# Optimization experiments

Hardware: AMD Instinct MI355X
Metric: run time of the kernel (lower is better)

## Reference

```python
import jax, jax.numpy as jnp
import numpy as np

B, N, H, F, DIN, NC = 4, 1024, 8, 256, 256, 10  # batch graphs, nodes, heads, feat/head, input dim, classes


def setup_inputs() -> dict:
    key = jax.random.key(0)
    ks = jax.random.split(key, 12)
    def rn(k, shape, s=0.05):
        return jax.random.normal(k, shape, jnp.float32) * s
    return dict(
        features=rn(ks[0], (B, N, DIN), 1.0),
        eigvects=rn(ks[1], (B, N, DIN), 1.0),  # unused by forward, mirrors original signature
        attn_mask=jnp.zeros((B, N, N), jnp.float32),  # additive mask: 0 = edge, -inf = no edge
        W1=rn(ks[2], (DIN, H * F)), a_src1=rn(ks[3], (H, F)), a_tgt1=rn(ks[4], (H, F)),
        skip1=rn(ks[5], (DIN, H * F)), b1=jnp.zeros((H * F,), jnp.float32),
        W2=rn(ks[6], (H * F, H * F)), a_src2=rn(ks[7], (H, F)), a_tgt2=rn(ks[8], (H, F)),
        skip2=rn(ks[9], (H * F, H * F)), b2=jnp.zeros((F,), jnp.float32),
        Wc=rn(ks[10], (F, NC)), bc=jnp.zeros((NC,), jnp.float32),
    )


def _gat_layer(x, mask, W, a_s, a_t, skipW, b, concat):
    # GAT IMP2: dense all-pairs scores + additive connectivity mask. Dropout is eval-mode identity.
    Bb, Nn, _ = x.shape
    Hh, Ff = a_s.shape
    p = (x @ W).reshape(Bb, Nn, Hh, Ff)                      # projected node features (B,N,H,F)
    s_src = jnp.einsum('bnhf,hf->bnh', p, a_s)
    s_tgt = jnp.einsum('bnhf,hf->bnh', p, a_t)
    # score[b,i,j,h] = leaky(src_i + tgt_j) + mask[b,i,j]
    scores = jax.nn.leaky_relu(s_src[:, :, None, :] + s_tgt[:, None, :, :], 0.2) + mask[..., None]
    attn = jax.nn.softmax(scores, axis=2)                    # softmax over neighbors j
    out = jnp.einsum('bijh,bjhf->bihf', attn, p)
    out = out + (x @ skipW).reshape(Bb, Nn, Hh, Ff)          # skip connection (projected)
    out = out.reshape(Bb, Nn, Hh * Ff) if concat else out.mean(axis=2)
    out = out + b
    return jax.nn.elu(out) if concat else out


def reference(features, eigvects, attn_mask, W1, a_src1, a_tgt1, skip1, b1,
              W2, a_src2, a_tgt2, skip2, b2, Wc, bc):
    x = _gat_layer(features, attn_mask, W1, a_src1, a_tgt1, skip1, b1, True)   # (B,N,H*F), ELU
    x = _gat_layer(x, attn_mask, W2, a_src2, a_tgt2, skip2, b2, False)         # (B,N,F), heads averaged
    g = x.mean(axis=1)                                                         # mean pool over nodes
    return g @ Wc + bc                                                         # (B, n_classes)
```

## Files before the change

### kernel.cpp

```cpp
#include <hip/hip_runtime.h>
#include <hip/hip_bf16.h>
#include <stdint.h>
#include <stddef.h>

typedef __hip_bfloat16 bf16;
typedef __attribute__((ext_vector_type(8))) short bhalf8;
typedef __attribute__((ext_vector_type(4))) short short4v;
typedef __attribute__((ext_vector_type(4))) float floatx4;

static __device__ __forceinline__ float b2f(bf16 v) { return __bfloat162float(v); }
static __device__ __forceinline__ bf16  f2b(float v) { return __float2bfloat16(v); }
static __device__ __forceinline__ short f2s(float v) {
    union { bf16 b; short s; } u; u.b = __float2bfloat16(v); return u.s;
}
static __device__ __forceinline__ float s2f(short v) {
    union { short s; bf16 b; } u; u.s = v; return b2f(u.b);
}

static __device__ __forceinline__ float loadf(const void* p, size_t i, int f32) {
    return f32 ? ((const float*)p)[i] : b2f(((const bf16*)p)[i]);
}

static __device__ __forceinline__ void gl_lds16(const void* g, void* l) {
    __builtin_amdgcn_global_load_lds(
        (const __attribute__((address_space(1))) void*)g,
        (__attribute__((address_space(3))) void*)l, 16, 0, 0);
}

static __device__ __forceinline__ void load_mask4b(const bf16* m, size_t idx,
                                                   float* mv) {
    short4v v = *(const short4v*)(m + idx);
    #pragma unroll
    for (int t = 0; t < 4; t++) mv[t] = s2f(v[t]);
}

__global__ __launch_bounds__(256) void prep_k(const void* __restrict__ feat,
                                              bf16* __restrict__ featc,
                                              const void* __restrict__ mask,
                                              bf16* __restrict__ maskb,
                                              float* __restrict__ zbase, int nzero,
                                              const void* __restrict__ W1,
                                              bf16* __restrict__ W1t,
                                              const void* __restrict__ skip1,
                                              bf16* __restrict__ S1t,
                                              const void* __restrict__ W2,
                                              const void* __restrict__ a_src1,
                                              const void* __restrict__ a_tgt1,
                                              const void* __restrict__ a_src2,
                                              const void* __restrict__ a_tgt2,
                                              bf16* __restrict__ Wa1b,
                                              bf16* __restrict__ Wa2b,
                                              int* __restrict__ flagp)
{
    __shared__ int sflag;
    __shared__ bf16 tile[32][33];
    const int tid = threadIdx.x;

    if (tid < 64) {
        const unsigned short* s = (const unsigned short*)W1;
        int bad = 0;
        #pragma unroll
        for (int i = 0; i < 4; i++) {
            int e = (s[tid * 4 + i] >> 7) & 0xFF;
            if (e > 0x85 || (e != 0 && e < 0x60)) bad++;
        }
        bad += __shfl_xor(bad, 1, 64);
        bad += __shfl_xor(bad, 2, 64);
        bad += __shfl_xor(bad, 4, 64);
        bad += __shfl_xor(bad, 8, 64);
        bad += __shfl_xor(bad, 16, 64);
        bad += __shfl_xor(bad, 32, 64);
        if (tid == 0) sflag = (bad > 16) ? 1 : 0;
    }
    __syncthreads();
    const int f32 = sflag;

    int id = blockIdx.x;
    if (id == 0 && tid == 0) *flagp = f32;

    if (id < 4096) {
        const int i = id * 256 + tid;
        featc[i] = f32 ? f2b(((const float*)feat)[i]) : ((const bf16*)feat)[i];
        return;
    }
    id -= 4096;
    if (id < 4096) {
        const size_t i = (size_t)id * 1024 + tid * 4;
        if (f32) {
            float4 v = *(const float4*)((const float*)mask + i);
            short4v o;
            o[0] = f2s(v.x); o[1] = f2s(v.y); o[2] = f2s(v.z); o[3] = f2s(v.w);
            *(short4v*)(maskb + i) = o;
        } else {
            *(short4v*)(maskb + i) = *(const short4v*)((const bf16*)mask + i);
        }
        return;
    }
    id -= 4096;
    if (id < 480) {
        const int i = id * 256 + tid;
        if (i < nzero) zbase[i] = 0.f;
        return;
    }
    id -= 480;
    if (id < 1024) {
        const void* in = (id < 512) ? W1 : skip1;
        bf16* out = (id < 512) ? W1t : S1t;
        const int t = id & 511;
        const int bx = t & 63, byy = t >> 6;
        const int tx = tid & 31, ty = tid >> 5;
        const int c0 = bx * 32, r0 = byy * 32;
        #pragma unroll
        for (int yy = ty; yy < 32; yy += 8)
            tile[yy][tx] = f2b(loadf(in, (size_t)(r0 + yy) * 2048 + c0 + tx, f32));
        __syncthreads();
        #pragma unroll
        for (int yy = ty; yy < 32; yy += 8)
            out[(size_t)(c0 + yy) * 256 + r0 + tx] = tile[tx][yy];
        return;
    }
    id -= 1024;
    if (id < 512) {
        const int wave = tid >> 6, lane = tid & 63;
        const int base = id * 64;
        const int hh = base >> 11, h = hh & 7;
        const void* a = (hh < 8) ? a_src2 : a_tgt2;
        float av[4];
        #pragma unroll
        for (int i = 0; i < 4; i++) av[i] = loadf(a, h * 256 + lane * 4 + i, f32);
        #pragma unroll 4
        for (int o = 0; o < 16; o++) {
            const int idx = base + wave * 16 + o;
            const int k = idx & 2047;
            float acc = 0.f;
            #pragma unroll
            for (int i = 0; i < 4; i++)
                acc = fmaf(loadf(W2, (size_t)k * 2048 + h * 256 + lane * 4 + i, f32),
                           av[i], acc);
            #pragma unroll
            for (int off2 = 32; off2; off2 >>= 1) acc += __shfl_down(acc, off2, 64);
            if (lane == 0) Wa2b[idx] = f2b(acc);
        }
        return;
    }
    id -= 512;
    {
        const int wave = tid >> 6, lane = tid & 63;
        const int base = id * 64;
        const int hh = base >> 8, h = hh & 7;
        const void* a = (hh < 8) ? a_src1 : a_tgt1;
        float av[4];
        #pragma unroll
        for (int i = 0; i < 4; i++) av[i] = loadf(a, h * 256 + lane * 4 + i, f32);
        #pragma unroll 4
        for (int o = 0; o < 16; o++) {
            const int idx = base + wave * 16 + o;
            const int k = idx & 255;
            float acc = 0.f;
            #pragma unroll
            for (int i = 0; i < 4; i++)
                acc = fmaf(loadf(W1, (size_t)k * 2048 + h * 256 + lane * 4 + i, f32),
                           av[i], acc);
            #pragma unroll
            for (int off2 = 32; off2; off2 >>= 1) acc += __shfl_down(acc, off2, 64);
            if (lane == 0) Wa1b[idx] = f2b(acc);
        }
    }
}

__global__ __launch_bounds__(256) void gemm_dual(const bf16* __restrict__ featc,
                                                 const bf16* __restrict__ W1t,
                                                 const bf16* __restrict__ S1t,
                                                 bf16* __restrict__ pT,
                                                 bf16* __restrict__ sk1)
{
    __shared__ __align__(16) short sA[128][32];
    __shared__ __align__(16) short sB[128][32];
    const int tid = threadIdx.x;
    const int z = blockIdx.z;
    const bf16* A  = z ? featc : W1t;
    const bf16* Bt = z ? S1t   : featc;
    const int mbase = (z ? blockIdx.x : blockIdx.y) * 128;
    const int nbase = (z ? blockIdx.y : blockIdx.x) * 128;
    const int wave = tid >> 6, lane = tid & 63;
    const int wm = wave >> 1, wn = wave & 1;
    const int lrow = lane & 15, quad = lane >> 4;

    floatx4 acc[4][4];
    #pragma unroll
    for (int i = 0; i < 4; i++)
        #pragma unroll
        for (int j = 0; j < 4; j++)
            acc[i][j] = (floatx4){0.f, 0.f, 0.f, 0.f};

    const int srow = wave * 32 + (lane >> 2);
    const int scol = (lane & 3) * 8;
    const bf16* gA0 = A  + (size_t)(mbase + srow) * 256 + scol;
    const bf16* gA1 = gA0 + (size_t)16 * 256;
    const bf16* gB0 = Bt + (size_t)(nbase + srow) * 256 + scol;
    const bf16* gB1 = gB0 + (size_t)16 * 256;
    char* lA0 = (char*)&sA[0][0] + wave * 2048 + lane * 16;
    char* lA1 = lA0 + 1024;
    char* lB0 = (char*)&sB[0][0] + wave * 2048 + lane * 16;
    char* lB1 = lB0 + 1024;

    for (int k0 = 0; k0 < 256; k0 += 32) {
        __syncthreads();
        gl_lds16(gA0 + k0, lA0);
        gl_lds16(gA1 + k0, lA1);
        gl_lds16(gB0 + k0, lB0);
        gl_lds16(gB1 + k0, lB1);
        __syncthreads();
        bhalf8 af[4], bfr[4];
        #pragma unroll
        for (int t = 0; t < 4; t++) af[t]  = *(const bhalf8*)&sA[wm * 64 + t * 16 + lrow][quad * 8];
        #pragma unroll
        for (int t = 0; t < 4; t++) bfr[t] = *(const bhalf8*)&sB[wn * 64 + t * 16 + lrow][quad * 8];
        #pragma unroll
        for (int tm = 0; tm < 4; tm++)
            #pragma unroll
            for (int tn = 0; tn < 4; tn++)
                acc[tm][tn] = __builtin_amdgcn_mfma_f32_16x16x32_bf16(af[tm], bfr[tn], acc[tm][tn], 0, 0, 0);
    }

    #pragma unroll
    for (int tm = 0; tm < 4; tm++) {
        #pragma unroll
        for (int tn = 0; tn < 4; tn++) {
            const int col = nbase + wn * 64 + tn * 16 + lrow;
            #pragma unroll
            for (int r = 0; r < 4; r++) {
                const int row = mbase + wm * 64 + tm * 16 + quad * 4 + r;
                if (z) {
                    sk1[(size_t)row * 2048 + col] = f2b(acc[tm][tn][r]);
                } else {
                    const size_t idx = ((size_t)((col >> 10) * 8 + (row >> 8)) << 18)
                                     + (size_t)(row & 255) * 1024 + (col & 1023);
                    pT[idx] = f2b(acc[tm][tn][r]);
                }
            }
        }
    }
}

template <int K>
__global__ __launch_bounds__(256) void score_k(const bf16* __restrict__ X,
                                               const bf16* __restrict__ Wab,
                                               float* __restrict__ ss,
                                               float* __restrict__ st)
{
    constexpr int VPL = K / 64;
    const int wave = threadIdx.x >> 6, lane = threadIdx.x & 63;
    const int n = blockIdx.x * 4 + wave;
    const int b = n >> 10, nn = n & 1023;

    const bf16* xr = X + (size_t)n * K + lane * VPL;
    float xv[VPL];
    if (VPL == 4) {
        short4v v = *(const short4v*)xr;
        #pragma unroll
        for (int t = 0; t < 4; t++) xv[t] = s2f(v[t]);
    } else {
        #pragma unroll
        for (int c = 0; c < VPL / 8; c++) {
            bhalf8 v = *(const bhalf8*)(xr + c * 8);
            #pragma unroll
            for (int t = 0; t < 8; t++) xv[c * 8 + t] = s2f(v[t]);
        }
    }

    #pragma unroll
    for (int hh = 0; hh < 16; hh++) {
        const bf16* wr = Wab + (size_t)hh * K + lane * VPL;
        float acc = 0.f;
        if (VPL == 4) {
            short4v v = *(const short4v*)wr;
            #pragma unroll
            for (int t = 0; t < 4; t++) acc = fmaf(xv[t], s2f(v[t]), acc);
        } else {
            #pragma unroll
            for (int c = 0; c < VPL / 8; c++) {
                bhalf8 v = *(const bhalf8*)(wr + c * 8);
                #pragma unroll
                for (int t = 0; t < 8; t++) acc = fmaf(xv[c * 8 + t], s2f(v[t]), acc);
            }
        }
        #pragma unroll
        for (int off = 32; off; off >>= 1) acc += __shfl_down(acc, off, 64);
        if (lane == 0) {
            const int h = hh & 7;
            if (hh < 8) ss[(b * 8 + h) * 1024 + nn] = acc;
            else        st[(b * 8 + h) * 1024 + nn] = acc;
        }
    }
}

__global__ __launch_bounds__(256) void attn_fused(const float* __restrict__ s_src_t,
                                                  const float* __restrict__ s_tgt_t,
                                                  const bf16* __restrict__ maskb,
                                                  const bf16* __restrict__ pT,
                                                  const bf16* __restrict__ sk,
                                                  const void* __restrict__ bias,
                                                  bf16* __restrict__ x2,
                                                  const int* __restrict__ flag)
{
    __shared__ __align__(16) short sA[2][64][32];
    __shared__ __align__(16) short sB[2][128][32];
    __shared__ short sStgt[1024];
    __shared__ float sInvl[64];

    const int tid = threadIdx.x;
    const int d = blockIdx.x;
    const int by = d & 15, fh = (d >> 4) & 1, bh = d >> 5;
    const int b = bh >> 3, h = bh & 7;
    const int f32 = *flag;
    const int wave = tid >> 6, lane = tid & 63;
    const int lrow = lane & 15, quad = lane >> 4;

    #pragma unroll
    for (int q = 0; q < 4; q++)
        sStgt[q * 256 + tid] = f2s(s_tgt_t[bh * 1024 + q * 256 + tid]);

    const int row  = tid >> 2;
    const int col0 = (tid & 3) * 8;
    const float ssr = s_src_t[bh * 1024 + by * 64 + row];
    const size_t mrow0 = ((size_t)(b * 1024 + by * 64 + row)) << 10;

    const bf16* gB = pT + ((size_t)bh << 18)
                   + (size_t)(fh * 128 + wave * 32 + (lane >> 2)) * 1024
                   + (lane & 3) * 8;

    floatx4 acc[4][2];
    #pragma unroll
    for (int i = 0; i < 4; i++)
        #pragma unroll
        for (int j = 0; j < 2; j++)
            acc[i][j] = (floatx4){0.f, 0.f, 0.f, 0.f};

    float lacc = 0.f;

    auto stageB = [&](int k0, int buf) {
        char* l = (char*)&sB[buf][0][0] + wave * 2048 + lane * 16;
        #pragma unroll
        for (int c = 0; c < 2; c++)
            gl_lds16(gB + (size_t)(c * 16) * 1024 + k0, l + c * 1024);
    };
    auto genA = [&](int k0, int buf, bhalf8 m8) {
        const short* sp = &sStgt[k0 + col0];
        bhalf8 ev;
        #pragma unroll
        for (int t = 0; t < 8; t++) {
            float x = ssr + s2f(sp[t]);
            x = fmaxf(x, 0.2f * x);
            float e = __expf(x + s2f(m8[t]));
            lacc += e;
            ev[t] = f2s(e);
        }
        *(bhalf8*)&sA[buf][row][col0] = ev;
    };
    auto loadmask = [&](int k0) -> bhalf8 {
        return *(const bhalf8*)(maskb + mrow0 + k0 + col0);
    };

    stageB(0, 0);
    bhalf8 mcur = loadmask(0);
    __syncthreads();
    genA(0, 0, mcur);
    bhalf8 mnxt = loadmask(32);

    int cur = 0;
    for (int k0 = 0; k0 < 1024; k0 += 32, cur ^= 1) {
        __syncthreads();
        if (k0 + 32 < 1024) {
            const int nxt = cur ^ 1;
            stageB(k0 + 32, nxt);
            genA(k0 + 32, nxt, mnxt);
            if (k0 + 64 < 1024)
                mnxt = loadmask(k0 + 64);
        }
        bhalf8 af[4], bfr[2];
        #pragma unroll
        for (int mt = 0; mt < 4; mt++)
            af[mt] = *(const bhalf8*)&sA[cur][mt * 16 + lrow][quad * 8];
        #pragma unroll
        for (int nt = 0; nt < 2; nt++)
            bfr[nt] = *(const bhalf8*)&sB[cur][wave * 32 + nt * 16 + lrow][quad * 8];
        #pragma unroll
        for (int mt = 0; mt < 4; mt++)
            #pragma unroll
            for (int nt = 0; nt < 2; nt++)
                acc[mt][nt] = __builtin_amdgcn_mfma_f32_16x16x32_bf16(af[mt], bfr[nt], acc[mt][nt], 0, 0, 0);
    }

    lacc += __shfl_xor(lacc, 1, 64);
    lacc += __shfl_xor(lacc, 2, 64);
    if ((tid & 3) == 0) sInvl[row] = 1.0f / lacc;
    __syncthreads();

    #pragma unroll
    for (int mt = 0; mt < 4; mt++) {
        #pragma unroll
        for (int r = 0; r < 4; r++) {
            const int rl = mt * 16 + quad * 4 + r;
            const int rg = by * 64 + rl;
            const float il = sInvl[rl];
            #pragma unroll
            for (int nt = 0; nt < 2; nt++) {
                const int col = fh * 128 + wave * 32 + nt * 16 + lrow;
                const int hf = h * 256 + col;
                const size_t idx = ((size_t)(b * 1024 + rg)) * 2048 + hf;
                float v = acc[mt][nt][r] * il + b2f(sk[idx]) + loadf(bias, hf, f32);
                v = (v > 0.f) ? v : expm1f(v);
                x2[idx] = f2b(v);
            }
        }
    }
}

__global__ __launch_bounds__(256) void colsoft_k(const float* __restrict__ s_src_t,
                                                 const float* __restrict__ s_tgt_t,
                                                 const bf16* __restrict__ maskb,
                                                 float* __restrict__ c)
{
    __shared__ float sS[64];
    __shared__ float sIl[64];
    const int bh = blockIdx.x, iz = blockIdx.y, b = bh >> 3;
    const int tid = threadIdx.x;
    const int i0 = iz * 64;
    if (tid < 64) sS[tid] = s_src_t[bh * 1024 + i0 + tid];
    __syncthreads();

    {
        const int row = tid >> 2, c4 = tid & 3;
        const float ssr = sS[row];
        const size_t mrow = ((size_t)(b * 1024 + i0 + row)) << 10;
        float l = 0.f;
        #pragma unroll 4
        for (int q = 0; q < 64; q++) {
            const int j = c4 * 256 + q * 4;
            float mv[4];
            load_mask4b(maskb, mrow + j, mv);
            float4 s4 = *(const float4*)(s_tgt_t + bh * 1024 + j);
            float sv[4] = {s4.x, s4.y, s4.z, s4.w};
            #pragma unroll
            for (int t = 0; t < 4; t++) {
                float x = ssr + sv[t];
                x = fmaxf(x, 0.2f * x);
                l += __expf(x + mv[t]);
            }
        }
        l += __shfl_xor(l, 1, 64);
        l += __shfl_xor(l, 2, 64);
        if ((tid & 3) == 0) sIl[row] = 1.0f / l;
    }
    __syncthreads();

    const int j0 = tid * 4;
    float4 s4 = *(const float4*)(s_tgt_t + bh * 1024 + j0);
    float sv[4] = {s4.x, s4.y, s4.z, s4.w};
    float a[4] = {0.f, 0.f, 0.f, 0.f};
    #pragma unroll 4
    for (int r = 0; r < 64; r++) {
        const float sr = sS[r], il = sIl[r];
        float mv[4];
        load_mask4b(maskb, (((size_t)(b * 1024 + i0 + r)) << 10) + j0, mv);
        #pragma unroll
        for (int t = 0; t < 4; t++) {
            float x = sr + sv[t];
            x = fmaxf(x, 0.2f * x);
            a[t] = fmaf(il, __expf(x + mv[t]), a[t]);
        }
    }
    #pragma unroll
    for (int t = 0; t < 4; t++)
        atomicAdd(&c[bh * 1024 + j0 + t], a[t]);
}

__global__ __launch_bounds__(256) void yx_k(const bf16* __restrict__ x2,
                                            const float* __restrict__ c,
                                            float* __restrict__ y,
                                            float* __restrict__ xbar)
{
    __shared__ float sC[8][32];
    const int b = blockIdx.x, kt = blockIdx.y, jc = blockIdx.z;
    const int t = threadIdx.x;
    const int k = kt * 512 + t * 2;
    const int j0 = jc * 32;
    {
        const int h = t >> 5, jj = t & 31;
        sC[h][jj] = c[(b * 8 + h) * 1024 + j0 + jj];
    }
    __syncthreads();
    float acc0[8] = {0.f, 0.f, 0.f, 0.f, 0.f, 0.f, 0.f, 0.f};
    float acc1[8] = {0.f, 0.f, 0.f, 0.f, 0.f, 0.f, 0.f, 0.f};
    float ax0 = 0.f, ax1 = 0.f;
    #pragma unroll 4
    for (int jj = 0; jj < 32; jj++) {
        const unsigned int v =
            *(const unsigned int*)&x2[((size_t)(b * 1024 + j0 + jj)) * 2048 + k];
        const float x0 = s2f((short)(v & 0xffff));
        const float x1 = s2f((short)(v >> 16));
        ax0 += x0; ax1 += x1;
        #pragma unroll
        for (int h = 0; h < 8; h++) {
            acc0[h] = fmaf(sC[h][jj], x0, acc0[h]);
            acc1[h] = fmaf(sC[h][jj], x1, acc1[h]);
        }
    }
    #pragma unroll
    for (int h = 0; h < 8; h++) {
        atomicAdd(&y[(b * 8 + h) * 2048 + k], acc0[h]);
        atomicAdd(&y[(b * 8 + h) * 2048 + k + 1], acc1[h]);
    }
    atomicAdd(&xbar[b * 2048 + k], ax0);
    atomicAdd(&xbar[b * 2048 + k + 1], ax1);
}

__global__ __launch_bounds__(256) void gs_k(const void* __restrict__ W2,
                                            const void* __restrict__ skip2,
                                            const float* __restrict__ y,
                                            const float* __restrict__ xbar,
                                            float* __restrict__ gA,
                                            float* __restrict__ gS,
                                            const int* __restrict__ flagp)
{
    __shared__ float sY[64];
    const int f32 = *flagp;
    int id = blockIdx.x;
    if (id < 1024) {
        const int bh = id & 31, kc = id >> 5;
        const int h = bh & 7, f = threadIdx.x;
        const int k0 = kc * 64;
        if (threadIdx.x < 64) sY[threadIdx.x] = y[bh * 2048 + k0 + threadIdx.x];
        __syncthreads();
        float acc = 0.f;
        #pragma unroll 4
        for (int kk = 0; kk < 64; kk++)
            acc = fmaf(sY[kk], loadf(W2, (size_t)(k0 + kk) * 2048 + h * 256 + f, f32), acc);
        atomicAdd(&gA[bh * 256 + f], acc);
    } else {
        const int idx = id - 1024;
        const int b = idx & 3, hft = (idx >> 2) & 7, kc = idx >> 5;
        const int hf = hft * 256 + threadIdx.x;
        const int k0 = kc * 64;
        if (threadIdx.x < 64) sY[threadIdx.x] = xbar[b * 2048 + k0 + threadIdx.x];
        __syncthreads();
        float acc = 0.f;
        #pragma unroll 4
        for (int kk = 0; kk < 64; kk++)
            acc = fmaf(sY[kk], loadf(skip2, (size_t)(k0 + kk) * 2048 + hf, f32), acc);
        atomicAdd(&gS[b * 2048 + hf], acc);
    }
}

__global__ __launch_bounds__(256) void classify2_k(const float* __restrict__ gA,
                                                   const float* __restrict__ gS,
                                                   const void* __restrict__ b2,
                                                   const void* __restrict__ Wc,
                                                   const void* __restrict__ bc,
                                                   void* __restrict__ out,
                                                   const int* __restrict__ flag)
{
    __shared__ float gv[256];
    const int f32 = *flag;
    const int b = blockIdx.x, f = threadIdx.x;
    float s = 0.f;
    #pragma unroll
    for (int h = 0; h < 8; h++)
        s += gA[(b * 8 + h) * 256 + f] + gS[b * 2048 + h * 256 + f];
    gv[f] = s * (1.0f / 8192.0f) + loadf(b2, f, f32);
    __syncthreads();
    if (f < 10) {
        float acc = loadf(bc, f, f32);
        for (int k = 0; k < 256; k++)
            acc = fmaf(gv[k], loadf(Wc, k * 10 + f, f32), acc);
        if (f32) ((float*)out)[b * 10 + f] = acc;
        else     ((bf16*)out)[b * 10 + f] = f2b(acc);
    }
}

extern "C" void kernel_launch(void* const* d_in, const int* in_sizes, int n_in,
                              void* d_out, int out_size, void* d_ws, size_t ws_size,
                              hipStream_t stream)
{
    (void)in_sizes; (void)n_in; (void)out_size; (void)ws_size;
    const void* feat   = d_in[0];
    const void* mask   = d_in[2];
    const void* W1     = d_in[3];
    const void* a_src1 = d_in[4];
    const void* a_tgt1 = d_in[5];
    const void* skip1  = d_in[6];
    const void* b1     = d_in[7];
    const void* W2     = d_in[8];
    const void* a_src2 = d_in[9];
    const void* a_tgt2 = d_in[10];
    const void* skip2  = d_in[11];
    const void* b2v    = d_in[12];
    const void* Wc     = d_in[13];
    const void* bc     = d_in[14];

    char* ws = (char*)d_ws;
    size_t off = 0;
    auto alloc = [&](size_t bytes) -> void* {
        void* p = ws + off;
        off += (bytes + 255) & ~(size_t)255;
        return p;
    };
    int*   flag  = (int*)alloc(256);
    bf16*  featc = (bf16*)alloc(4096ull * 256 * 2);
    bf16*  maskb = (bf16*)alloc(4ull * 1024 * 1024 * 2);
    bf16*  W1t   = (bf16*)alloc(2048ull * 256 * 2);
    bf16*  S1t   = (bf16*)alloc(2048ull * 256 * 2);
    bf16*  sk1   = (bf16*)alloc(4096ull * 2048 * 2);
    bf16*  x2    = (bf16*)alloc(4096ull * 2048 * 2);
    bf16*  pT    = (bf16*)alloc(4096ull * 2048 * 2);
    float* ss    = (float*)alloc(32ull * 1024 * 4);
    float* st    = (float*)alloc(32ull * 1024 * 4);
    bf16*  Wa1b  = (bf16*)alloc(16ull * 256 * 2);
    bf16*  Wa2b  = (bf16*)alloc(16ull * 2048 * 2);
    float* cbuf = (float*)alloc(32ull * 1024 * 4);
    float* gA   = (float*)alloc(32ull * 256 * 4);
    float* gS   = (float*)alloc(4ull * 2048 * 4);
    float* xbar = (float*)alloc(4ull * 2048 * 4);
    float* y    = (float*)alloc(32ull * 2048 * 4);
    const int nzero = 32768 + 3 * 8192 + 65536;

    prep_k<<<10272, 256, 0, stream>>>(feat, featc, mask, maskb, cbuf, nzero,
                                      W1, W1t, skip1, S1t, W2,
                                      a_src1, a_tgt1, a_src2, a_tgt2,
                                      Wa1b, Wa2b, flag);
    gemm_dual<<<dim3(32, 16, 2), 256, 0, stream>>>(featc, W1t, S1t, pT, sk1);
    score_k<256><<<1024, 256, 0, stream>>>(featc, Wa1b, ss, st);
    attn_fused<<<1024, 256, 0, stream>>>(ss, st, maskb, pT, sk1, b1, x2, flag);
    score_k<2048><<<1024, 256, 0, stream>>>(x2, Wa2b, ss, st);
    colsoft_k<<<dim3(32, 16), 256, 0, stream>>>(ss, st, maskb, cbuf);
    yx_k<<<dim3(4, 4, 32), 256, 0, stream>>>(x2, cbuf, y, xbar);
    gs_k<<<2048, 256, 0, stream>>>(W2, skip2, y, xbar, gA, gS, flag);
    classify2_k<<<4, 256, 0, stream>>>(gA, gS, b2v, Wc, bc, d_out, flag);
}
```

Baseline: 352.2 us.

## Split column softmax into row-sum and column-sum kernels sharing mask across heads

Replaces the per-(batch,head) colsoft kernel with two kernels: one computes softmax denominators for all 8 heads per mask tile, the other accumulates column weights for all heads. Each mask element is then read once per batch instead of once per head. The yx kernel now handles 128 nodes per block instead of 32, and gs_k processes all 4 batches per weight load, so there are fewer atomics and fewer redundant reads of the weights. The cost is an extra launch, an extra zeroed buffer, and fewer blocks in yx_k and gs_k.

```diff
diff --git a/kernel.cpp b/kernel.cpp
--- a/kernel.cpp
+++ b/kernel.cpp
@@ -97,12 +97,12 @@
         return;
     }
     id -= 4096;
-    if (id < 480) {
+    if (id < 608) {
         const int i = id * 256 + tid;
         if (i < nzero) zbase[i] = 0.f;
         return;
     }
-    id -= 480;
+    id -= 608;
     if (id < 1024) {
         const void* in = (id < 512) ? W1 : skip1;
         bf16* out = (id < 512) ? W1t : S1t;
@@ -417,63 +417,113 @@
     }
 }
 
-__global__ __launch_bounds__(256) void colsoft_k(const float* __restrict__ s_src_t,
-                                                 const float* __restrict__ s_tgt_t,
-                                                 const bf16* __restrict__ maskb,
-                                                 float* __restrict__ c)
-{
-    __shared__ float sS[64];
-    __shared__ float sIl[64];
-    const int bh = blockIdx.x, iz = blockIdx.y, b = bh >> 3;
+__global__ __launch_bounds__(256) void lsum_k(const float* __restrict__ ss,
+                                              const float* __restrict__ st,
+                                              const bf16* __restrict__ maskb,
+                                              float* __restrict__ lbuf)
+{
+    __shared__ float sSt[8][256];
+    __shared__ float sPart[4][64];
+    const int b = blockIdx.x, iz = blockIdx.y, jq = blockIdx.z;
     const int tid = threadIdx.x;
-    const int i0 = iz * 64;
-    if (tid < 64) sS[tid] = s_src_t[bh * 1024 + i0 + tid];
+    const int w = tid >> 6, lane = tid & 63;
+    const int i0 = iz * 64, j0 = jq * 256;
+
+    #pragma unroll
+    for (int t = 0; t < 8; t++) {
+        const int idx = t * 256 + tid;
+        const int h = idx >> 8, j = idx & 255;
+        sSt[h][j] = st[(b * 8 + h) * 1024 + j0 + j];
+    }
+
+    bhalf8 mreg[8];
+    const bf16* mrow = maskb + (((size_t)(b * 1024 + i0 + lane)) << 10) + j0 + w * 64;
+    #pragma unroll
+    for (int c = 0; c < 8; c++) mreg[c] = *(const bhalf8*)(mrow + c * 8);
+
     __syncthreads();
 
-    {
-        const int row = tid >> 2, c4 = tid & 3;
-        const float ssr = sS[row];
-        const size_t mrow = ((size_t)(b * 1024 + i0 + row)) << 10;
-        float l = 0.f;
-        #pragma unroll 4
-        for (int q = 0; q < 64; q++) {
-            const int j = c4 * 256 + q * 4;
-            float mv[4];
-            load_mask4b(maskb, mrow + j, mv);
-            float4 s4 = *(const float4*)(s_tgt_t + bh * 1024 + j);
-            float sv[4] = {s4.x, s4.y, s4.z, s4.w};
-            #pragma unroll
-            for (int t = 0; t < 4; t++) {
-                float x = ssr + sv[t];
+    float lh[8];
+    #pragma unroll
+    for (int h = 0; h < 8; h++) {
+        const float ssr = ss[(b * 8 + h) * 1024 + i0 + lane];
+        float acc = 0.f;
+        #pragma unroll
+        for (int c = 0; c < 8; c++) {
+            #pragma unroll
+            for (int t = 0; t < 8; t++) {
+                float x = ssr + sSt[h][w * 64 + c * 8 + t];
                 x = fmaxf(x, 0.2f * x);
-                l += __expf(x + mv[t]);
+                acc += __expf(x + s2f(mreg[c][t]));
             }
         }
-        l += __shfl_xor(l, 1, 64);
-        l += __shfl_xor(l, 2, 64);
-        if ((tid & 3) == 0) sIl[row] = 1.0f / l;
-    }
+        lh[h] = acc;
+    }
+
+    #pragma unroll
+    for (int h = 0; h < 8; h++) {
+        __syncthreads();
+        sPart[w][lane] = lh[h];
+        __syncthreads();
+        if (w == 0)
+            atomicAdd(&lbuf[(b * 8 + h) * 1024 + i0 + lane],
+                      sPart[0][lane] + sPart[1][lane] + sPart[2][lane] + sPart[3][lane]);
+    }
+}
+
+__global__ __launch_bounds__(256) void csum_k(const float* __restrict__ ss,
+                                              const float* __restrict__ st,
+                                              const bf16* __restrict__ maskb,
+                                              const float* __restrict__ lbuf,
+                                              float* __restrict__ c)
+{
+    __shared__ float sSS[8][256];
+    __shared__ float sIl[8][256];
+    __shared__ float sC[4][8][64];
+    const int b = blockIdx.x, jz = blockIdx.y, iq = blockIdx.z;
+    const int tid = threadIdx.x;
+    const int w = tid >> 6, lane = tid & 63;
+    const int j0 = jz * 64, i0 = iq * 256;
+
+    #pragma unroll
+    for (int t = 0; t < 8; t++) {
+        const int idx = t * 256 + tid;
+        const int h = idx >> 8, ii = idx & 255;
+        sSS[h][ii] = ss[(b * 8 + h) * 1024 + i0 + ii];
+        sIl[h][ii] = 1.0f / lbuf[(b * 8 + h) * 1024 + i0 + ii];
+    }
+
+    float stj[8];
+    #pragma unroll
+    for (int h = 0; h < 8; h++)
+        stj[h] = st[(b * 8 + h) * 1024 + j0 + lane];
+
+    float accc[8] = {0.f, 0.f, 0.f, 0.f, 0.f, 0.f, 0.f, 0.f};
     __syncthreads();
 
-    const int j0 = tid * 4;
-    float4 s4 = *(const float4*)(s_tgt_t + bh * 1024 + j0);
-    float sv[4] = {s4.x, s4.y, s4.z, s4.w};
-    float a[4] = {0.f, 0.f, 0.f, 0.f};
-    #pragma unroll 4
-    for (int r = 0; r < 64; r++) {
-        const float sr = sS[r], il = sIl[r];
-        float mv[4];
-        load_mask4b(maskb, (((size_t)(b * 1024 + i0 + r)) << 10) + j0, mv);
-        #pragma unroll
-        for (int t = 0; t < 4; t++) {
-            float x = sr + sv[t];
+    const short* mp = (const short*)maskb
+                    + (((size_t)(b * 1024 + i0 + w * 64)) << 10) + j0 + lane;
+    #pragma unroll 2
+    for (int ii = 0; ii < 64; ii++) {
+        const float m = s2f(mp[(size_t)ii << 10]);
+        const int il = w * 64 + ii;
+        #pragma unroll
+        for (int h = 0; h < 8; h++) {
+            float x = sSS[h][il] + stj[h];
             x = fmaxf(x, 0.2f * x);
-            a[t] = fmaf(il, __expf(x + mv[t]), a[t]);
-        }
-    }
-    #pragma unroll
-    for (int t = 0; t < 4; t++)
-        atomicAdd(&c[bh * 1024 + j0 + t], a[t]);
+            accc[h] = fmaf(__expf(x + m), sIl[h][il], accc[h]);
+        }
+    }
+
+    #pragma unroll
+    for (int h = 0; h < 8; h++) sC[w][h][lane] = accc[h];
+    __syncthreads();
+    if (w == 0) {
+        #pragma unroll
+        for (int h = 0; h < 8; h++)
+            atomicAdd(&c[(b * 8 + h) * 1024 + j0 + lane],
+                      sC[0][h][lane] + sC[1][h][lane] + sC[2][h][lane] + sC[3][h][lane]);
+    }
 }
 
 __global__ __launch_bounds__(256) void yx_k(const bf16* __restrict__ x2,
@@ -481,21 +531,22 @@
                                             float* __restrict__ y,
                                             float* __restrict__ xbar)
 {
-    __shared__ float sC[8][32];
+    __shared__ float sC[8][128];
     const int b = blockIdx.x, kt = blockIdx.y, jc = blockIdx.z;
     const int t = threadIdx.x;
     const int k = kt * 512 + t * 2;
-    const int j0 = jc * 32;
-    {
-        const int h = t >> 5, jj = t & 31;
-        sC[h][jj] = c[(b * 8 + h) * 1024 + j0 + jj];
+    const int j0 = jc * 128;
+    #pragma unroll
+    for (int q = 0; q < 4; q++) {
+        const int idx = q * 256 + t;
+        sC[idx >> 7][idx & 127] = c[(b * 8 + (idx >> 7)) * 1024 + j0 + (idx & 127)];
     }
     __syncthreads();
     float acc0[8] = {0.f, 0.f, 0.f, 0.f, 0.f, 0.f, 0.f, 0.f};
     float acc1[8] = {0.f, 0.f, 0.f, 0.f, 0.f, 0.f, 0.f, 0.f};
     float ax0 = 0.f, ax1 = 0.f;
     #pragma unroll 4
-    for (int jj = 0; jj < 32; jj++) {
+    for (int jj = 0; jj < 128; jj++) {
         const unsigned int v =
             *(const unsigned int*)&x2[((size_t)(b * 1024 + j0 + jj)) * 2048 + k];
         const float x0 = s2f((short)(v & 0xffff));
@@ -524,32 +575,42 @@
                                             float* __restrict__ gS,
                                             const int* __restrict__ flagp)
 {
-    __shared__ float sY[64];
+    __shared__ float sY[4][64];
     const int f32 = *flagp;
-    int id = blockIdx.x;
-    if (id < 1024) {
-        const int bh = id & 31, kc = id >> 5;
-        const int h = bh & 7, f = threadIdx.x;
-        const int k0 = kc * 64;
-        if (threadIdx.x < 64) sY[threadIdx.x] = y[bh * 2048 + k0 + threadIdx.x];
+    const int id = blockIdx.x;
+    const int tid = threadIdx.x;
+    const int bq = tid >> 6, kk6 = tid & 63;
+    if (id < 256) {
+        const int h = id & 7, kc = id >> 3;
+        const int k0 = kc * 64, f = tid;
+        sY[bq][kk6] = y[(bq * 8 + h) * 2048 + k0 + kk6];
         __syncthreads();
-        float acc = 0.f;
+        float a[4] = {0.f, 0.f, 0.f, 0.f};
         #pragma unroll 4
-        for (int kk = 0; kk < 64; kk++)
-            acc = fmaf(sY[kk], loadf(W2, (size_t)(k0 + kk) * 2048 + h * 256 + f, f32), acc);
-        atomicAdd(&gA[bh * 256 + f], acc);
+        for (int kk = 0; kk < 64; kk++) {
+            const float wv = loadf(W2, (size_t)(k0 + kk) * 2048 + h * 256 + f, f32);
+            #pragma unroll
+            for (int bb = 0; bb < 4; bb++) a[bb] = fmaf(sY[bb][kk], wv, a[bb]);
+        }
+        #pragma unroll
+        for (int bb = 0; bb < 4; bb++)
+            atomicAdd(&gA[(bb * 8 + h) * 256 + f], a[bb]);
     } else {
-        const int idx = id - 1024;
-        const int b = idx & 3, hft = (idx >> 2) & 7, kc = idx >> 5;
-        const int hf = hft * 256 + threadIdx.x;
-        const int k0 = kc * 64;
-        if (threadIdx.x < 64) sY[threadIdx.x] = xbar[b * 2048 + k0 + threadIdx.x];
+        const int idq = id - 256;
+        const int hft = idq & 7, kc = idq >> 3;
+        const int k0 = kc * 64, hf = hft * 256 + tid;
+        sY[bq][kk6] = xbar[bq * 2048 + k0 + kk6];
         __syncthreads();
-        float acc = 0.f;
+        float a[4] = {0.f, 0.f, 0.f, 0.f};
         #pragma unroll 4
-        for (int kk = 0; kk < 64; kk++)
-            acc = fmaf(sY[kk], loadf(skip2, (size_t)(k0 + kk) * 2048 + hf, f32), acc);
-        atomicAdd(&gS[b * 2048 + hf], acc);
+        for (int kk = 0; kk < 64; kk++) {
+            const float sv = loadf(skip2, (size_t)(k0 + kk) * 2048 + hf, f32);
+            #pragma unroll
+            for (int bb = 0; bb < 4; bb++) a[bb] = fmaf(sY[bb][kk], sv, a[bb]);
+        }
+        #pragma unroll
+        for (int bb = 0; bb < 4; bb++)
+            atomicAdd(&gS[bb * 2048 + hf], a[bb]);
     }
 }
 
@@ -623,9 +684,10 @@
     float* gS   = (float*)alloc(4ull * 2048 * 4);
     float* xbar = (float*)alloc(4ull * 2048 * 4);
     float* y    = (float*)alloc(32ull * 2048 * 4);
-    const int nzero = 32768 + 3 * 8192 + 65536;
-
-    prep_k<<<10272, 256, 0, stream>>>(feat, featc, mask, maskb, cbuf, nzero,
+    float* lbuf = (float*)alloc(32ull * 1024 * 4);
+    const int nzero = 32768 + 3 * 8192 + 65536 + 32768;
+
+    prep_k<<<10400, 256, 0, stream>>>(feat, featc, mask, maskb, cbuf, nzero,
                                       W1, W1t, skip1, S1t, W2,
                                       a_src1, a_tgt1, a_src2, a_tgt2,
                                       Wa1b, Wa2b, flag);
@@ -633,8 +695,9 @@
     score_k<256><<<1024, 256, 0, stream>>>(featc, Wa1b, ss, st);
     attn_fused<<<1024, 256, 0, stream>>>(ss, st, maskb, pT, sk1, b1, x2, flag);
     score_k<2048><<<1024, 256, 0, stream>>>(x2, Wa2b, ss, st);
-    colsoft_k<<<dim3(32, 16), 256, 0, stream>>>(ss, st, maskb, cbuf);
-    yx_k<<<dim3(4, 4, 32), 256, 0, stream>>>(x2, cbuf, y, xbar);
-    gs_k<<<2048, 256, 0, stream>>>(W2, skip2, y, xbar, gA, gS, flag);
+    lsum_k<<<dim3(4, 16, 4), 256, 0, stream>>>(ss, st, maskb, lbuf);
+    csum_k<<<dim3(4, 16, 4), 256, 0, stream>>>(ss, st, maskb, lbuf, cbuf);
+    yx_k<<<dim3(4, 4, 8), 256, 0, stream>>>(x2, cbuf, y, xbar);
+    gs_k<<<512, 256, 0, stream>>>(W2, skip2, y, xbar, gA, gS, flag);
     classify2_k<<<4, 256, 0, stream>>>(gA, gS, b2v, Wc, bc, d_out, flag);
 }
```

Measured after the change: 374.0 us. +6.2%, slower.

## Widen attention tile to full head width and batch gs_k over graphs

Applied to the files above, without the earlier changes.

The fused attention kernel now has each block compute all 256 feature columns for its 64 rows instead of half, so the exp/leaky-relu score tile (genA) and mask loads happen once per row block rather than twice. The grid halves to 512 blocks, and each wave holds a 4x4 MFMA accumulator tile with a doubled B staging buffer in LDS. Separately, gs_k now processes all four batch graphs per block, so each W2/skip2 weight element is loaded once and reused for four FMAs, cutting weight traffic fourfold and the block count to 512. The cost is more registers and LDS per block and fewer blocks to fill the GPU, which may lower occupancy.

```diff
diff --git a/kernel.cpp b/kernel.cpp
--- a/kernel.cpp
+++ b/kernel.cpp
@@ -305,13 +305,13 @@
                                                   const int* __restrict__ flag)
 {
     __shared__ __align__(16) short sA[2][64][32];
-    __shared__ __align__(16) short sB[2][128][32];
+    __shared__ __align__(16) short sB[2][256][32];
     __shared__ short sStgt[1024];
     __shared__ float sInvl[64];
 
     const int tid = threadIdx.x;
     const int d = blockIdx.x;
-    const int by = d & 15, fh = (d >> 4) & 1, bh = d >> 5;
+    const int by = d & 15, bh = d >> 4;
     const int b = bh >> 3, h = bh & 7;
     const int f32 = *flag;
     const int wave = tid >> 6, lane = tid & 63;
@@ -327,22 +327,22 @@
     const size_t mrow0 = ((size_t)(b * 1024 + by * 64 + row)) << 10;
 
     const bf16* gB = pT + ((size_t)bh << 18)
-                   + (size_t)(fh * 128 + wave * 32 + (lane >> 2)) * 1024
+                   + (size_t)(wave * 64 + (lane >> 2)) * 1024
                    + (lane & 3) * 8;
 
-    floatx4 acc[4][2];
+    floatx4 acc[4][4];
     #pragma unroll
     for (int i = 0; i < 4; i++)
         #pragma unroll
-        for (int j = 0; j < 2; j++)
+        for (int j = 0; j < 4; j++)
             acc[i][j] = (floatx4){0.f, 0.f, 0.f, 0.f};
 
     float lacc = 0.f;
 
     auto stageB = [&](int k0, int buf) {
-        char* l = (char*)&sB[buf][0][0] + wave * 2048 + lane * 16;
-        #pragma unroll
-        for (int c = 0; c < 2; c++)
+        char* l = (char*)&sB[buf][0][0] + wave * 4096 + lane * 16;
+        #pragma unroll
+        for (int c = 0; c < 4; c++)
             gl_lds16(gB + (size_t)(c * 16) * 1024 + k0, l + c * 1024);
     };
     auto genA = [&](int k0, int buf, bhalf8 m8) {
@@ -378,17 +378,17 @@
             if (k0 + 64 < 1024)
                 mnxt = loadmask(k0 + 64);
         }
-        bhalf8 af[4], bfr[2];
+        bhalf8 af[4], bfr[4];
         #pragma unroll
         for (int mt = 0; mt < 4; mt++)
             af[mt] = *(const bhalf8*)&sA[cur][mt * 16 + lrow][quad * 8];
         #pragma unroll
-        for (int nt = 0; nt < 2; nt++)
-            bfr[nt] = *(const bhalf8*)&sB[cur][wave * 32 + nt * 16 + lrow][quad * 8];
+        for (int nt = 0; nt < 4; nt++)
+            bfr[nt] = *(const bhalf8*)&sB[cur][wave * 64 + nt * 16 + lrow][quad * 8];
         #pragma unroll
         for (int mt = 0; mt < 4; mt++)
             #pragma unroll
-            for (int nt = 0; nt < 2; nt++)
+            for (int nt = 0; nt < 4; nt++)
                 acc[mt][nt] = __builtin_amdgcn_mfma_f32_16x16x32_bf16(af[mt], bfr[nt], acc[mt][nt], 0, 0, 0);
     }
 
@@ -405,8 +405,8 @@
             const int rg = by * 64 + rl;
             const float il = sInvl[rl];
             #pragma unroll
-            for (int nt = 0; nt < 2; nt++) {
-                const int col = fh * 128 + wave * 32 + nt * 16 + lrow;
+            for (int nt = 0; nt < 4; nt++) {
+                const int col = wave * 64 + nt * 16 + lrow;
                 const int hf = h * 256 + col;
                 const size_t idx = ((size_t)(b * 1024 + rg)) * 2048 + hf;
                 float v = acc[mt][nt][r] * il + b2f(sk[idx]) + loadf(bias, hf, f32);
@@ -524,32 +524,42 @@
                                             float* __restrict__ gS,
                                             const int* __restrict__ flagp)
 {
-    __shared__ float sY[64];
+    __shared__ float sY[4][64];
     const int f32 = *flagp;
-    int id = blockIdx.x;
-    if (id < 1024) {
-        const int bh = id & 31, kc = id >> 5;
-        const int h = bh & 7, f = threadIdx.x;
-        const int k0 = kc * 64;
-        if (threadIdx.x < 64) sY[threadIdx.x] = y[bh * 2048 + k0 + threadIdx.x];
+    const int id = blockIdx.x;
+    const int tid = threadIdx.x;
+    const int bq = tid >> 6, kk6 = tid & 63;
+    if (id < 256) {
+        const int h = id & 7, kc = id >> 3;
+        const int k0 = kc * 64, f = tid;
+        sY[bq][kk6] = y[(bq * 8 + h) * 2048 + k0 + kk6];
         __syncthreads();
-        float acc = 0.f;
+        float a[4] = {0.f, 0.f, 0.f, 0.f};
         #pragma unroll 4
-        for (int kk = 0; kk < 64; kk++)
-            acc = fmaf(sY[kk], loadf(W2, (size_t)(k0 + kk) * 2048 + h * 256 + f, f32), acc);
-        atomicAdd(&gA[bh * 256 + f], acc);
+        for (int kk = 0; kk < 64; kk++) {
+            const float wv = loadf(W2, (size_t)(k0 + kk) * 2048 + h * 256 + f, f32);
+            #pragma unroll
+            for (int bb = 0; bb < 4; bb++) a[bb] = fmaf(sY[bb][kk], wv, a[bb]);
+        }
+        #pragma unroll
+        for (int bb = 0; bb < 4; bb++)
+            atomicAdd(&gA[(bb * 8 + h) * 256 + f], a[bb]);
     } else {
-        const int idx = id - 1024;
-        const int b = idx & 3, hft = (idx >> 2) & 7, kc = idx >> 5;
-        const int hf = hft * 256 + threadIdx.x;
-        const int k0 = kc * 64;
-        if (threadIdx.x < 64) sY[threadIdx.x] = xbar[b * 2048 + k0 + threadIdx.x];
+        const int idq = id - 256;
+        const int hft = idq & 7, kc = idq >> 3;
+        const int k0 = kc * 64, hf = hft * 256 + tid;
+        sY[bq][kk6] = xbar[bq * 2048 + k0 + kk6];
         __syncthreads();
-        float acc = 0.f;
+        float a[4] = {0.f, 0.f, 0.f, 0.f};
         #pragma unroll 4
-        for (int kk = 0; kk < 64; kk++)
-            acc = fmaf(sY[kk], loadf(skip2, (size_t)(k0 + kk) * 2048 + hf, f32), acc);
-        atomicAdd(&gS[b * 2048 + hf], acc);
+        for (int kk = 0; kk < 64; kk++) {
+            const float sv = loadf(skip2, (size_t)(k0 + kk) * 2048 + hf, f32);
+            #pragma unroll
+            for (int bb = 0; bb < 4; bb++) a[bb] = fmaf(sY[bb][kk], sv, a[bb]);
+        }
+        #pragma unroll
+        for (int bb = 0; bb < 4; bb++)
+            atomicAdd(&gS[bb * 2048 + hf], a[bb]);
     }
 }
 
@@ -631,10 +641,10 @@
                                       Wa1b, Wa2b, flag);
     gemm_dual<<<dim3(32, 16, 2), 256, 0, stream>>>(featc, W1t, S1t, pT, sk1);
     score_k<256><<<1024, 256, 0, stream>>>(featc, Wa1b, ss, st);
-    attn_fused<<<1024, 256, 0, stream>>>(ss, st, maskb, pT, sk1, b1, x2, flag);
+    attn_fused<<<512, 256, 0, stream>>>(ss, st, maskb, pT, sk1, b1, x2, flag);
     score_k<2048><<<1024, 256, 0, stream>>>(x2, Wa2b, ss, st);
     colsoft_k<<<dim3(32, 16), 256, 0, stream>>>(ss, st, maskb, cbuf);
     yx_k<<<dim3(4, 4, 32), 256, 0, stream>>>(x2, cbuf, y, xbar);
-    gs_k<<<2048, 256, 0, stream>>>(W2, skip2, y, xbar, gA, gS, flag);
+    gs_k<<<512, 256, 0, stream>>>(W2, skip2, y, xbar, gA, gS, flag);
     classify2_k<<<4, 256, 0, stream>>>(gA, gS, b2v, Wc, bc, d_out, flag);
 }
```

New measurement: 360.6 us. +2.4%, slower.
